# Kernel optimization log

Hardware: AMD Instinct MI355X
Metric: run time of the kernel (lower is better)

Reference implementation:

```python
import jax, jax.numpy as jnp
import numpy as np
from jax.scipy.special import logsumexp

N, D, M = 131072, 32, 256


def setup_inputs() -> dict:
    key = jax.random.key(0)
    k1, k2, k3 = jax.random.split(key, 3)
    X = jax.random.normal(k1, (N, D), dtype=jnp.float32)
    center = jax.random.uniform(k2, (M, D), dtype=jnp.float32)
    # cov_inv_sqrt near identity so det(cov_inv) ~ 1 (fit() would init it via Cholesky);
    # random-matrix init would make det overflow/underflow.
    cov_inv_sqrt = (jnp.eye(D, dtype=jnp.float32)[None, :, :]
                    + 0.02 * jax.random.normal(k3, (M, D, D), dtype=jnp.float32))
    weight = jnp.ones((M,), dtype=jnp.float32)
    threshold = jnp.zeros((1,), dtype=jnp.float32)
    return {"X": X, "center": center, "cov_inv_sqrt": cov_inv_sqrt,
            "weight": weight, "threshold": threshold}


def reference(X, center, cov_inv_sqrt, weight, threshold):
    # refresh(): equal_clusters=True branch
    w = jnp.abs(weight)
    pr = w / w.sum()                                            # [M]
    cov_inv = jnp.einsum('mij,mkj->mik', cov_inv_sqrt, cov_inv_sqrt)  # L L^T, [M,D,D]
    coef = pr * jnp.sqrt(jnp.linalg.det(cov_inv))               # [M]

    # Mahalanobis: q_ij = (x_i - c_j)^T A_j (x_i - c_j), expanded to avoid [N,M,D]:
    #   q_ij = xx_i . A_j_flat - 2 x_i . (A_j c_j) + c_j^T A_j c_j
    n, d = X.shape
    m = center.shape[0]
    A_flat = cov_inv.reshape(m, d * d)                          # [M, D*D]
    xx = (X[:, :, None] * X[:, None, :]).reshape(n, d * d)      # [N, D*D]
    term1 = xx @ A_flat.T                                       # [N, M]
    Ac = jnp.einsum('mkl,ml->mk', cov_inv, center)              # [M, D]
    term2 = X @ Ac.T                                            # [N, M]
    term3 = jnp.einsum('mk,mk->m', center, Ac)                  # [M]
    d_ij = -0.5 * (term1 - 2.0 * term2 + term3[None, :])        # [N, M]

    # weighted logsumexp over clusters: log sum_j coef_j exp(d_ij)
    ll = logsumexp(d_ij, axis=1, b=coef[None, :])               # [N]
    return ll - threshold[0]
```

## Files before the change

### kernel.cpp

```cpp
#include <hip/hip_runtime.h>
#include <hip/hip_bf16.h>
#include <math.h>

#define NPTS 131072
#define DIM 32
#define MCL 256
#define NSTEP 18
#define BPTS 128
#define THREADS 256

typedef __attribute__((ext_vector_type(8))) _Float16 f16x8;
typedef __attribute__((ext_vector_type(2))) _Float16 h2v;
typedef __attribute__((ext_vector_type(2))) unsigned u2v;
typedef __attribute__((ext_vector_type(4))) float f32x4;

__device__ __forceinline__ short f2h(float f) {
    _Float16 h = (_Float16)f;
    union { _Float16 h; short s; } X; X.h = h; return X.s;
}

__global__ __launch_bounds__(256) void gmm_prep(
    const float* __restrict__ center,
    const float* __restrict__ L,
    const float* __restrict__ weight,
    short* __restrict__ G,
    float* __restrict__ cst)
{
    const int m = blockIdx.x;
    const int t = threadIdx.x;
    __shared__ float Ls[DIM][DIM + 1];
    __shared__ float As[DIM][DIM + 1];
    __shared__ float Acs[DIM];
    __shared__ float red[DIM];

    const float* Lm = L + m * DIM * DIM;
    for (int k = t; k < DIM * DIM; k += 256)
        Ls[k >> 5][k & 31] = Lm[k];
    __syncthreads();

    for (int idx = t; idx < DIM * DIM; idx += 256) {
        const int j = idx >> 5, l = idx & 31;
        float a = 0.f;
        #pragma unroll
        for (int d = 0; d < DIM; ++d) a = fmaf(Ls[j][d], Ls[l][d], a);
        As[j][l] = a;
    }
    __syncthreads();

    if (t < DIM) {
        float a = 0.f;
        #pragma unroll
        for (int l = 0; l < DIM; ++l) a = fmaf(As[t][l], center[m * DIM + l], a);
        Acs[t] = a;
        red[t] = a * center[m * DIM + t];
    }
    __syncthreads();

    const int mt = m >> 4, ml = m & 15;
    for (int idx = t; idx < NSTEP * 32; idx += 256) {
        const int s = idx >> 5, k = idx & 31;
        float c;
        if (s == 0)       c = As[k][k] - 1.0f;
        else if (s <= 15) c = 2.0f * As[k][(k + s) & 31];
        else if (s == 16) c = (k < 16) ? 2.0f * As[k][k + 16] : -2.0f * Acs[k - 16];
        else              c = (k < 16) ? -2.0f * Acs[k + 16] : 0.0f;
        G[s * 8192 + mt * 512 + (k >> 3) * 128 + ml * 8 + (k & 7)] = f2h(c);
    }

    if (t < 64) {
        float logdet = 0.f;
        if (t < DIM) {
            float col[DIM];
            #pragma unroll
            for (int r2 = 0; r2 < DIM; ++r2) col[r2] = Ls[r2][t];
            float prodabs = 1.0f;
            #pragma unroll
            for (int k = 0; k < DIM; ++k) {
                const float pv  = __shfl(col[k], k, 64);
                const float rpv = 1.0f / pv;
                const float cjk = col[k];
                #pragma unroll
                for (int t2 = k + 1; t2 < DIM; ++t2) {
                    const float f = __shfl(col[t2], k, 64) * rpv;
                    col[t2] = fmaf(-f, cjk, col[t2]);
                }
                prodabs *= fabsf(pv);
            }
            logdet = logf(prodabs);
        }

        float wsp = 0.f;
        for (int j = t; j < MCL; j += 64) wsp += fabsf(weight[j]);
        #pragma unroll
        for (int d2 = 1; d2 < 64; d2 <<= 1) wsp += __shfl_xor(wsp, d2, 64);

        if (t == 0) {
            float t3 = 0.f;
            #pragma unroll
            for (int j = 0; j < DIM; ++j) t3 += red[j];
            cst[m] = logf(fabsf(weight[m])) - logf(wsp) + logdet - 0.5f * t3;
        }
    }
}

template<int J>
__device__ __forceinline__ unsigned wword(const u2v b0, const u2v b1, const u2v b2) {
    if constexpr (J < 2)      return b0[J];
    else if constexpr (J < 4) return b1[J - 2];
    else                      return b2[J - 4];
}

template<int OFF2, int Q>
__device__ __forceinline__ h2v wpair(const u2v b0, const u2v b1, const u2v b2) {
    static_assert((OFF2 & 1) == 0, "odd offsets eliminated by XhO copy");
    constexpr int wj = (OFF2 + 2 * Q) >> 1;
    union { unsigned u; h2v h; } X; X.u = wword<wj>(b0, b1, b2); return X.h;
}

template<int S, int Q, int OFF2>
__device__ __forceinline__ h2v mkpair(const h2v (&xp)[4], int kg,
                                      const u2v b0, const u2v b1, const u2v b2) {
    if constexpr (S == 0) {
        return xp[Q] * xp[Q];
    } else {
        const h2v wp = wpair<OFF2, Q>(b0, b1, b2);
        if constexpr (S == 16) {
            return (kg < 2) ? (h2v)(xp[Q] * wp) : wp;
        } else if constexpr (S == 17) {
            const h2v z = { (_Float16)0.f, (_Float16)0.f };
            return (kg < 2) ? wp : z;
        } else {
            return xp[Q] * wp;
        }
    }
}

template<int S>
__device__ __forceinline__ void k_step(
    const short* __restrict__ gw,
    const short* __restrict__ Xh,
    const short* __restrict__ XhO,
    const int (&rowh)[4],
    const h2v (&xp)[4][4],
    f16x8 (&bf)[8],
    f32x4 (&acc)[4][8],
    int kg)
{
    constexpr int shv  = (S == 17) ? 16 : S;
    constexpr bool odd = (shv & 1) != 0;
    constexpr int sh2  = odd ? (shv - 1) : shv;
    constexpr int off2 = sh2 & 3;
    const int bq = ((kg * 8 + sh2) & 31) & ~3;

    f16x8 af[4];
    #pragma unroll
    for (int i = 0; i < 4; ++i) {
        u2v b0 = {}, b1 = {}, b2 = {};
        if constexpr (S != 0) {
            const short* xr = (odd ? XhO : Xh) + rowh[i] + bq;
            b0 = *(const u2v*)(xr);
            b1 = *(const u2v*)(xr + 4);
            if constexpr (off2 != 0) b2 = *(const u2v*)(xr + 8);
        }
        union { f16x8 v; h2v p[4]; } U;
        U.p[0] = mkpair<S, 0, off2>(xp[i], kg, b0, b1, b2);
        U.p[1] = mkpair<S, 1, off2>(xp[i], kg, b0, b1, b2);
        U.p[2] = mkpair<S, 2, off2>(xp[i], kg, b0, b1, b2);
        U.p[3] = mkpair<S, 3, off2>(xp[i], kg, b0, b1, b2);
        af[i] = U.v;
    }

    #pragma unroll
    for (int j = 0; j < 8; ++j) {
        #pragma unroll
        for (int i = 0; i < 4; ++i)
            acc[i][j] = __builtin_amdgcn_mfma_f32_16x16x32_f16(
                af[i], bf[j], acc[i][j], 0, 0, 0);
        if constexpr (S + 1 < NSTEP)
            bf[j] = *(const f16x8*)(gw + (size_t)(S + 1) * 8192 + j * 512);
    }
    __builtin_amdgcn_sched_barrier(0x107);
}

template<int S>
__device__ __forceinline__ void k_loop(
    const short* __restrict__ gw, const short* __restrict__ Xh,
    const short* __restrict__ XhO,
    const int (&rowh)[4], const h2v (&xp)[4][4],
    f16x8 (&bf)[8], f32x4 (&acc)[4][8], int kg)
{
    k_step<S>(gw, Xh, XhO, rowh, xp, bf, acc, kg);
    if constexpr (S + 1 < NSTEP)
        k_loop<S + 1>(gw, Xh, XhO, rowh, xp, bf, acc, kg);
}

__global__ __launch_bounds__(THREADS, 2) void gmm_mfma(
    const float* __restrict__ X,
    const short* __restrict__ G,
    const float* __restrict__ cstw,
    const float* __restrict__ thr,
    float* __restrict__ out)
{
    __shared__ __attribute__((aligned(16))) short Xh[BPTS * 44];
    __shared__ __attribute__((aligned(16))) short XhO[BPTS * 44];
    __shared__ float nrm_s[BPTS];
    __shared__ float cst_s[MCL];
    __shared__ float lse_m[BPTS];
    __shared__ float lse_d[BPTS];

    const int tid  = threadIdx.x;
    const int lane = tid & 63;
    const int w    = tid >> 6;
    const int wr   = w & 1;
    const int wc   = w >> 1;
    const int r    = lane & 15;
    const int kg   = lane >> 4;
    const int P0   = blockIdx.x * BPTS;

    const short* gw = G + wc * 4096 + lane * 8;

    int rowh[4];
    h2v xp[4][4];
    #pragma unroll
    for (int i = 0; i < 4; ++i) {
        const int row = wr * 64 + i * 16 + r;
        rowh[i] = row * 44;
        const float4* xg = reinterpret_cast<const float4*>(
            X + (size_t)(P0 + row) * DIM + kg * 8);
        const float4 a = xg[0], b = xg[1];
        xp[i][0] = h2v{ (_Float16)a.x, (_Float16)a.y };
        xp[i][1] = h2v{ (_Float16)a.z, (_Float16)a.w };
        xp[i][2] = h2v{ (_Float16)b.x, (_Float16)b.y };
        xp[i][3] = h2v{ (_Float16)b.z, (_Float16)b.w };
    }

    {
        const int p = tid >> 1, hf = tid & 1;
        const float4* Xg = reinterpret_cast<const float4*>(
            X + (size_t)(P0 + p) * DIM + hf * 16);
        float part = 0.f;
        #pragma unroll
        for (int q = 0; q < 4; ++q) {
            const float4 v = Xg[q];
            const int kb = hf * 16 + 4 * q;
            const short h0 = f2h(v.x), h1 = f2h(v.y), h2 = f2h(v.z), h3 = f2h(v.w);
            Xh[p * 44 + kb + 0] = h0;
            Xh[p * 44 + kb + 1] = h1;
            Xh[p * 44 + kb + 2] = h2;
            Xh[p * 44 + kb + 3] = h3;
            if (!hf && q < 2) {
                Xh[p * 44 + 32 + kb + 0] = h0;
                Xh[p * 44 + 32 + kb + 1] = h1;
                Xh[p * 44 + 32 + kb + 2] = h2;
                Xh[p * 44 + 32 + kb + 3] = h3;
            }
            const int i0 = (kb - 1) & 31;
            XhO[p * 44 + i0] = h0;
            XhO[p * 44 + kb + 0] = h1;
            XhO[p * 44 + kb + 1] = h2;
            XhO[p * 44 + kb + 2] = h3;
            if (i0 < 8)       XhO[p * 44 + 32 + i0] = h0;
            if (kb + 0 < 8) { XhO[p * 44 + 32 + kb + 0] = h1; }
            if (kb + 1 < 8) { XhO[p * 44 + 32 + kb + 1] = h2; }
            if (kb + 2 < 8) { XhO[p * 44 + 32 + kb + 2] = h3; }
            part = fmaf(v.x, v.x, part); part = fmaf(v.y, v.y, part);
            part = fmaf(v.z, v.z, part); part = fmaf(v.w, v.w, part);
        }
        part += __shfl_xor(part, 1, 64);
        if (!hf) nrm_s[p] = part;
        cst_s[tid] = cstw[tid];
    }

    f16x8 bf[8];
    #pragma unroll
    for (int j = 0; j < 8; ++j)
        bf[j] = *(const f16x8*)(gw + j * 512);

    __syncthreads();

    f32x4 acc[4][8] = {};
    k_loop<0>(gw, Xh, XhO, rowh, xp, bf, acc, kg);

    float cstr[8];
    #pragma unroll
    for (int j = 0; j < 8; ++j)
        cstr[j] = cst_s[wc * 128 + j * 16 + r];

    float mx[16], sm[16];
    #pragma unroll
    for (int i = 0; i < 4; ++i)
        #pragma unroll
        for (int rg = 0; rg < 4; ++rg) {
            const int sl = i * 4 + rg;
            float m_ = -1e30f;
            #pragma unroll
            for (int j = 0; j < 8; ++j)
                m_ = fmaxf(m_, fmaf(acc[i][j][rg], -0.5f, cstr[j]));
            #pragma unroll
            for (int d = 1; d < 16; d <<= 1)
                m_ = fmaxf(m_, __shfl_xor(m_, d, 64));
            float s_ = 0.f;
            #pragma unroll
            for (int j = 0; j < 8; ++j)
                s_ += __expf(fmaf(acc[i][j][rg], -0.5f, cstr[j]) - m_);
            #pragma unroll
            for (int d = 1; d < 16; d <<= 1)
                s_ += __shfl_xor(s_, d, 64);
            mx[sl] = m_; sm[sl] = s_;
        }

    if (wc == 0 && r == 0) {
        #pragma unroll
        for (int i = 0; i < 4; ++i)
            #pragma unroll
            for (int rg = 0; rg < 4; ++rg) {
                const int p2 = wr * 64 + i * 16 + kg * 4 + rg;
                lse_m[p2] = mx[i * 4 + rg];
                lse_d[p2] = sm[i * 4 + rg];
            }
    }
    __syncthreads();
    if (wc == 1 && r == 0) {
        const float thrv = thr[0];
        #pragma unroll
        for (int i = 0; i < 4; ++i)
            #pragma unroll
            for (int rg = 0; rg < 4; ++rg) {
                const int sl = i * 4 + rg;
                const int p2 = wr * 64 + i * 16 + kg * 4 + rg;
                const float om = lse_m[p2], os = lse_d[p2];
                const float nm = fmaxf(mx[sl], om);
                const float ss = sm[sl] * __expf(mx[sl] - nm) + os * __expf(om - nm);
                out[P0 + p2] = nm + __logf(ss) - 0.5f * nrm_s[p2] - thrv;
            }
    }
}

extern "C" void kernel_launch(void* const* d_in, const int* in_sizes, int n_in,
                              void* d_out, int out_size, void* d_ws, size_t ws_size,
                              hipStream_t stream)
{
    const float* X      = (const float*)d_in[0];
    const float* center = (const float*)d_in[1];
    const float* L      = (const float*)d_in[2];
    const float* weight = (const float*)d_in[3];
    const float* thr    = (const float*)d_in[4];
    float* out = (float*)d_out;

    float* cst = (float*)d_ws;
    short* G   = (short*)((char*)d_ws + 1024);

    gmm_prep<<<MCL, 256, 0, stream>>>(center, L, weight, G, cst);
    gmm_mfma<<<NPTS / BPTS, THREADS, 0, stream>>>(X, G, cst, thr, out);
}
```

Baseline: 68.01 us.

## Stage cluster weight tiles through double-buffered LDS with direct global-to-LDS loads

Rather than each wave loading its B fragments straight from global memory into registers, the block cooperatively stages each K-step's 8192-element weight tile into a double-buffered LDS region using global_load_lds. The next step is prefetched while the current one computes, and a barrier follows each step. The aim is to share B loads across the two row waves and cut redundant global traffic and register pressure. The cost is 32KB of extra LDS, which may reduce occupancy, plus a full-block barrier per step that serializes the waves.

Result: slower. 72.24 us (+6.2%).

```diff
diff --git a/kernel.cpp b/kernel.cpp
--- a/kernel.cpp
+++ b/kernel.cpp
@@ -17,6 +17,12 @@
 __device__ __forceinline__ short f2h(float f) {
     _Float16 h = (_Float16)f;
     union { _Float16 h; short s; } X; X.h = h; return X.s;
+}
+
+__device__ __forceinline__ void glds16(const void* g, void* l) {
+    __builtin_amdgcn_global_load_lds(
+        (const __attribute__((address_space(1))) unsigned int*)g,
+        (__attribute__((address_space(3))) unsigned int*)l, 16, 0, 0);
 }
 
 __global__ __launch_bounds__(256) void gmm_prep(
@@ -136,16 +142,30 @@
 }
 
 template<int S>
+__device__ __forceinline__ void stage(const short* __restrict__ G,
+                                      short (&Bb)[2][8192], int w, int lane)
+{
+    constexpr int b = S & 1;
+    const short* gs = G + (size_t)S * 8192 + w * 2048 + lane * 8;
+    #pragma unroll
+    for (int q = 0; q < 4; ++q)
+        glds16(gs + q * 512, &Bb[b][w * 2048 + q * 512]);
+}
+
+template<int S>
 __device__ __forceinline__ void k_step(
-    const short* __restrict__ gw,
+    const short* __restrict__ G,
+    short (&Bb)[2][8192],
     const short* __restrict__ Xh,
     const short* __restrict__ XhO,
     const int (&rowh)[4],
     const h2v (&xp)[4][4],
-    f16x8 (&bf)[8],
     f32x4 (&acc)[4][8],
-    int kg)
-{
+    int w, int lane, int kg, int wc)
+{
+    constexpr int cb = S & 1;
+    if constexpr (S + 1 < NSTEP) stage<S + 1>(G, Bb, w, lane);
+
     constexpr int shv  = (S == 17) ? 16 : S;
     constexpr bool odd = (shv & 1) != 0;
     constexpr int sh2  = odd ? (shv - 1) : shv;
@@ -170,28 +190,32 @@
         af[i] = U.v;
     }
 
-    #pragma unroll
-    for (int j = 0; j < 8; ++j) {
-        #pragma unroll
-        for (int i = 0; i < 4; ++i)
+    f16x8 bf[8];
+    #pragma unroll
+    for (int j = 0; j < 8; ++j)
+        bf[j] = *(const f16x8*)&Bb[cb][(wc * 8 + j) * 512 + lane * 8];
+
+    #pragma unroll
+    for (int i = 0; i < 4; ++i)
+        #pragma unroll
+        for (int j = 0; j < 8; ++j)
             acc[i][j] = __builtin_amdgcn_mfma_f32_16x16x32_f16(
                 af[i], bf[j], acc[i][j], 0, 0, 0);
-        if constexpr (S + 1 < NSTEP)
-            bf[j] = *(const f16x8*)(gw + (size_t)(S + 1) * 8192 + j * 512);
-    }
-    __builtin_amdgcn_sched_barrier(0x107);
+
+    if constexpr (S + 1 < NSTEP)
+        asm volatile("s_waitcnt vmcnt(0) lgkmcnt(0)\n\ts_barrier" ::: "memory");
 }
 
 template<int S>
 __device__ __forceinline__ void k_loop(
-    const short* __restrict__ gw, const short* __restrict__ Xh,
-    const short* __restrict__ XhO,
+    const short* __restrict__ G, short (&Bb)[2][8192],
+    const short* __restrict__ Xh, const short* __restrict__ XhO,
     const int (&rowh)[4], const h2v (&xp)[4][4],
-    f16x8 (&bf)[8], f32x4 (&acc)[4][8], int kg)
-{
-    k_step<S>(gw, Xh, XhO, rowh, xp, bf, acc, kg);
+    f32x4 (&acc)[4][8], int w, int lane, int kg, int wc)
+{
+    k_step<S>(G, Bb, Xh, XhO, rowh, xp, acc, w, lane, kg, wc);
     if constexpr (S + 1 < NSTEP)
-        k_loop<S + 1>(gw, Xh, XhO, rowh, xp, bf, acc, kg);
+        k_loop<S + 1>(G, Bb, Xh, XhO, rowh, xp, acc, w, lane, kg, wc);
 }
 
 __global__ __launch_bounds__(THREADS, 2) void gmm_mfma(
@@ -201,6 +225,7 @@
     const float* __restrict__ thr,
     float* __restrict__ out)
 {
+    __shared__ __attribute__((aligned(16))) short Bb[2][8192];
     __shared__ __attribute__((aligned(16))) short Xh[BPTS * 44];
     __shared__ __attribute__((aligned(16))) short XhO[BPTS * 44];
     __shared__ float nrm_s[BPTS];
@@ -217,7 +242,7 @@
     const int kg   = lane >> 4;
     const int P0   = blockIdx.x * BPTS;
 
-    const short* gw = G + wc * 4096 + lane * 8;
+    stage<0>(G, Bb, w, lane);
 
     int rowh[4];
     h2v xp[4][4];
@@ -271,15 +296,10 @@
         cst_s[tid] = cstw[tid];
     }
 
-    f16x8 bf[8];
-    #pragma unroll
-    for (int j = 0; j < 8; ++j)
-        bf[j] = *(const f16x8*)(gw + j * 512);
-
-    __syncthreads();
+    asm volatile("s_waitcnt vmcnt(0) lgkmcnt(0)\n\ts_barrier" ::: "memory");
 
     f32x4 acc[4][8] = {};
-    k_loop<0>(gw, Xh, XhO, rowh, xp, bf, acc, kg);
+    k_loop<0>(G, Bb, Xh, XhO, rowh, xp, acc, w, lane, kg, wc);
 
     float cstr[8];
     #pragma unroll
```
